# Performance work log

Measured on AMD Instinct MI355X. Metric: run time of the kernel, lower is better.

The kernel has to match this reference:

```python
import jax, jax.numpy as jnp
import numpy as np
from jax import lax

H = 128          # hidden_size
D = 8            # input_size
GX, GY = 4, 4    # grid_size
C = GX * GY      # grid cells
NS = 4.0         # neighborhood_size
T = 15           # obs_len
N = 16384        # neighbors per frame


def setup_inputs() -> dict:
    key = jax.random.key(0)
    ks = jax.random.split(key, 30)
    def w(i, shape):
        return jax.random.normal(ks[i], shape, jnp.float32) * 0.05
    return {
        "observed_trajectory_target": jax.random.normal(ks[0], (T, D), jnp.float32),
        "observed_trajectory_others": jax.random.normal(ks[1], (T, N, D), jnp.float32),
        "neighbor_mask": jax.random.randint(ks[2], (T, N), 0, 2, dtype=jnp.int32),
        "W_ih": w(3, (4 * H, D)), "W_hh": w(4, (4 * H, H)),
        "b_ih": w(5, (4 * H,)), "b_hh": w(6, (4 * H,)),
        "Wq": w(7, (H, H)), "bq": w(8, (H,)),
        "Wk": w(9, (H, H)), "bk": w(10, (H,)),
        "Wv": w(11, (H, H)), "bv": w(12, (H,)),
        "Wo": w(13, (H, H)), "bo": w(14, (H,)),
        "Wgq": w(15, (H, H)), "bgq": w(16, (H,)),
        "Wgk": w(17, (H, H)), "bgk": w(18, (H,)),
        "Wgv": w(19, (H, H)), "bgv": w(20, (H,)),
        "Wc": w(21, (2, H)), "bc": w(22, (2,)),
    }


def _lstm_cell(x, h, c, W_ih, W_hh, b_ih, b_hh):
    # torch LSTMCell gate order: i, f, g, o
    g = x @ W_ih.T + b_ih + h @ W_hh.T + b_hh
    i, f, gg, o = jnp.split(g, 4, axis=-1)
    c2 = jax.nn.sigmoid(f) * c + jax.nn.sigmoid(i) * jnp.tanh(gg)
    h2 = jax.nn.sigmoid(o) * jnp.tanh(c2)
    return h2, c2


def _forward(target, others, mask, W_ih, W_hh, b_ih, b_hh, Wq, bq, Wk, bk, Wv, bv,
             Wo, bo, Wgq, bgq, Wgk, bgk, Wgv, bgv, Wc, bc):
    # Neighbor LSTM is re-initialized to zero every timestep in the original
    # -> single LSTM step from zero state, vectorized over [T, N].
    g = jnp.einsum('tnd,kd->tnk', others, W_ih) + b_ih + b_hh
    i, f, gg, o = jnp.split(g, 4, axis=-1)
    c_o = jax.nn.sigmoid(i) * jnp.tanh(gg)
    h_others = jax.nn.sigmoid(o) * jnp.tanh(c_o)          # [T, N, H]

    scale = 1.0 / jnp.sqrt(jnp.asarray(H, jnp.float32))
    half = NS / 2.0
    cw, ch = NS / GX, NS / GY
    cells = jnp.arange(C, dtype=jnp.int32)

    def step(carry, xs):
        h, c = carry
        xt, ho, pos, mk = xs                               # [D], [N,H], [N,2], [N]
        h, c = _lstm_cell(xt[None, :], h, c, W_ih, W_hh, b_ih, b_hh)  # [1,H]
        # --- dynamic grid binning (trunc-toward-zero matches torch .long()) ---
        rel = pos - xt[:2]                                 # [N,2]
        in_nb = (jnp.abs(rel[:, 0]) <= half) & (jnp.abs(rel[:, 1]) <= half)
        cx = jnp.trunc(rel[:, 0] / cw).astype(jnp.int32) + GX // 2
        cy = jnp.trunc(rel[:, 1] / ch).astype(jnp.int32) + GY // 2
        valid = in_nb & (cx >= 0) & (cx < GX) & (cy >= 0) & (cy < GY) & (mk != 0)
        idx = cy * GX + cx                                 # [N]
        member = (idx[None, :] == cells[:, None]) & valid[None, :]  # [C,N]
        # --- per-cell single-query attention (1-head MHA) ---
        q = h @ Wq.T + bq                                  # [1,H]
        k = ho @ Wk.T + bk                                 # [N,H]
        v = ho @ Wv.T + bv                                 # [N,H]
        sc = (q @ k.T)[0] * scale                          # [N]
        mx = jnp.max(jnp.where(member, sc[None, :], -1e30), axis=1, keepdims=True)
        e = jnp.where(member, jnp.exp(sc[None, :] - mx), 0.0)
        w = e / jnp.maximum(e.sum(axis=1, keepdims=True), 1e-30)  # [C,N]
        nonempty = member.any(axis=1)                      # [C]
        cell_out = (w @ v) @ Wo.T + bo                     # [C,H]
        cell_out = jnp.where(nonempty[:, None], cell_out, 0.0)  # empty cells -> exact zeros
        # --- grid-level attention over the C cell summaries ---
        K = cell_out @ Wgk.T + bgk                         # [C,H]
        V = cell_out @ Wgv.T + bgv                         # [C,H]
        qg = h @ Wgq.T + bgq                               # [1,H]
        gw = jax.nn.softmax((qg @ K.T) * scale, axis=-1)   # [1,C]
        ctx = gw @ V                                       # [1,H]
        combined = h + ctx                                 # [1,H]
        return (h, c), combined

    h0 = jnp.zeros((1, H), jnp.float32)
    c0 = jnp.zeros((1, H), jnp.float32)
    _, ys = lax.scan(step, (h0, c0),
                     (target, h_others, others[..., :2], mask))
    combined = ys[-1][None]                                # [1,1,H] (matches torch broadcast)
    return combined @ Wc.T + bc                            # [1,1,2]


def reference(observed_trajectory_target, observed_trajectory_others, neighbor_mask,
              W_ih, W_hh, b_ih, b_hh, Wq, bq, Wk, bk, Wv, bv, Wo, bo,
              Wgq, bgq, Wgk, bgk, Wgv, bgv, Wc, bc):
    return _forward(observed_trajectory_target, observed_trajectory_others, neighbor_mask,
                    W_ih, W_hh, b_ih, b_hh, Wq, bq, Wk, bk, Wv, bv, Wo, bo,
                    Wgq, bgq, Wgk, bgk, Wgv, bgv, Wc, bc)
```

## Files before the change

### kernel.cpp

```cpp
#include <hip/hip_runtime.h>
#include <math.h>

#define WS_H     0
#define WS_U     128
#define WS_W2    256
#define WS_QBK   384
#define WS_S0    385
#define WS_S1    386
#define WS_GUARD 400
#define WS_ACCR  512
#define REP_STRIDE 2064
#define NREP 4

__device__ __forceinline__ float frcp_(float x){ return __builtin_amdgcn_rcpf(x); }
__device__ __forceinline__ float fsig_(float x){ return frcp_(1.f + __expf(-x)); }
__device__ __forceinline__ float ftanh_(float x){ return 1.f - 2.f*frcp_(1.f + __expf(2.f*x)); }

__device__ __forceinline__ float pf_(const float* __restrict__ p, int n, int part, int tid) {
    const int per4 = n >> 7;
    const float4* p4 = (const float4*)p + part * per4;
    float a = 0.f;
    for (int i = tid; i < per4; i += 256) { float4 v = p4[i]; a += v.x + v.y + v.z + v.w; }
    return a;
}

__global__ __launch_bounds__(256) void k0_prefetch(
    const float* __restrict__ W_ih, const float* __restrict__ W_hh,
    const float* __restrict__ Wq,  const float* __restrict__ Wk,
    const float* __restrict__ Wv,  const float* __restrict__ Wo,
    const float* __restrict__ Wgq, const float* __restrict__ Wgk,
    const float* __restrict__ Wgv, const float* __restrict__ Wc,
    float* __restrict__ ws)
{
    const int tid = threadIdx.x;
    const int bid = blockIdx.x;
    if (bid == 0) {
        for (int i = tid; i < NREP * REP_STRIDE; i += 256) ws[WS_ACCR + i] = 0.f;
    }
    const int part = bid >> 3;
    float a = pf_(W_hh, 65536, part, tid);
    a += pf_(W_ih, 4096,  part, tid);
    a += pf_(Wq,  16384, part, tid);
    a += pf_(Wk,  16384, part, tid);
    a += pf_(Wv,  16384, part, tid);
    a += pf_(Wo,  16384, part, tid);
    a += pf_(Wgq, 16384, part, tid);
    a += pf_(Wgk, 16384, part, tid);
    a += pf_(Wgv, 16384, part, tid);
    if (part < 2) a += pf_(Wc, 256, part, tid);
    if (a == 1.0e38f) ws[WS_GUARD] = a;
}

__global__ __launch_bounds__(512, 2) void k1_target(
    const float* __restrict__ target,
    const float* __restrict__ W_ih, const float* __restrict__ W_hh,
    const float* __restrict__ b_ih, const float* __restrict__ b_hh,
    const float* __restrict__ Wq,  const float* __restrict__ bq,
    const float* __restrict__ Wk,  const float* __restrict__ bk,
    const float* __restrict__ Wv,  const float* __restrict__ bv,
    const float* __restrict__ Wo,  const float* __restrict__ bo,
    const float* __restrict__ Wgq, const float* __restrict__ bgq,
    const float* __restrict__ Wgk, const float* __restrict__ bgk,
    float* __restrict__ ws)
{
    __shared__ __align__(16) float h_s[128];
    __shared__ float g_s[512];
    __shared__ float red[512];
    __shared__ __align__(16) float qq_s[256];
    __shared__ __align__(16) float u_s[128], ug_s[128], w1_s[128], w2_s[128];
    const int tid = threadIdx.x;
    if (tid < 128) h_s[tid] = 0.f;

    float wih[8];
    #pragma unroll
    for (int k = 0; k < 8; ++k) wih[k] = W_ih[tid*8 + k];
    const float bsum = b_ih[tid] + b_hh[tid];
    float4 whh[32];
    {
        const float4* w4 = (const float4*)(W_hh + tid*128);
        #pragma unroll
        for (int m = 0; m < 32; ++m) whh[m] = w4[m];
    }
    float c = 0.f;
    __syncthreads();

    for (int t = 0; t < 15; ++t) {
        float g = bsum;
        #pragma unroll
        for (int k = 0; k < 8; ++k) g += target[t*8 + k] * wih[k];
        const float4* h4 = (const float4*)h_s;
        float a0 = 0.f, a1 = 0.f, a2 = 0.f, a3 = 0.f;
        #pragma unroll
        for (int m = 0; m < 32; m += 4) {
            float4 x0 = h4[m], x1 = h4[m+1], x2 = h4[m+2], x3 = h4[m+3];
            a0 += whh[m  ].x*x0.x + whh[m  ].y*x0.y + whh[m  ].z*x0.z + whh[m  ].w*x0.w;
            a1 += whh[m+1].x*x1.x + whh[m+1].y*x1.y + whh[m+1].z*x1.z + whh[m+1].w*x1.w;
            a2 += whh[m+2].x*x2.x + whh[m+2].y*x2.y + whh[m+2].z*x2.z + whh[m+2].w*x2.w;
            a3 += whh[m+3].x*x3.x + whh[m+3].y*x3.y + whh[m+3].z*x3.z + whh[m+3].w*x3.w;
        }
        g += (a0 + a1) + (a2 + a3);
        g_s[tid] = g;
        __syncthreads();
        if (tid < 128) {
            float ig = fsig_(g_s[tid]);
            float fg = fsig_(g_s[tid+128]);
            float gg = ftanh_(g_s[tid+256]);
            float og = fsig_(g_s[tid+384]);
            c = fg*c + ig*gg;
            h_s[tid] = og*ftanh_(c);
        }
        __syncthreads();
    }

    {
        const int o = tid & 255, p = tid >> 8;
        const float* Wrow = (o < 128) ? (Wq + o*128) : (Wgq + (o & 127)*128);
        const float4* w4 = (const float4*)Wrow + p*16;
        const float4* h4 = (const float4*)h_s + p*16;
        float a = 0.f;
        #pragma unroll
        for (int m = 0; m < 16; ++m) { float4 w = w4[m], v = h4[m];
            a += w.x*v.x + w.y*v.y + w.z*v.z + w.w*v.w; }
        red[tid] = a;
    }
    __syncthreads();
    if (tid < 256) qq_s[tid] = red[tid] + red[tid+256] + ((tid < 128) ? bq[tid] : bgq[tid & 127]);
    __syncthreads();
    {
        const int o = tid & 255, p = tid >> 8;
        const int a_ = o & 127;
        const float* W = (o < 128) ? Wk : Wgk;
        const int qb = (o < 128) ? 0 : 128;
        float a = 0.f;
        #pragma unroll 8
        for (int j = p*64; j < p*64 + 64; ++j) a += qq_s[qb + j] * W[j*128 + a_];
        red[tid] = a;
    }
    __syncthreads();
    if (tid < 256) {
        float v = red[tid] + red[tid+256];
        if (tid < 128) u_s[tid] = v; else ug_s[tid & 127] = v;
    }
    __syncthreads();
    {
        const int o = tid & 127, p = tid >> 7;
        float a = 0.f;
        #pragma unroll 8
        for (int j = p*32; j < p*32 + 32; ++j) a += ug_s[j] * Wo[j*128 + o];
        red[tid] = a;
    }
    __syncthreads();
    if (tid < 128) w1_s[tid] = red[tid] + red[tid+128] + red[tid+256] + red[tid+384];
    __syncthreads();
    {
        const int o = tid & 127, p = tid >> 7;
        float a = 0.f;
        #pragma unroll 8
        for (int j = p*32; j < p*32 + 32; ++j) a += w1_s[j] * Wv[j*128 + o];
        red[tid] = a;
    }
    __syncthreads();
    if (tid < 128) w2_s[tid] = red[tid] + red[tid+128] + red[tid+256] + red[tid+384];
    __syncthreads();
    if (tid < 128) {
        red[tid]     = qq_s[tid] * bk[tid];
        red[128+tid] = qq_s[128+tid] * bgk[tid];
        red[256+tid] = w1_s[tid]*bv[tid] + ug_s[tid]*bo[tid];
    }
    __syncthreads();
    if (tid == 0) {
        float qbk = 0.f, s0 = 0.f, sx = 0.f;
        for (int j = 0; j < 128; ++j) { qbk += red[j]; s0 += red[128+j]; sx += red[256+j]; }
        ws[WS_QBK] = qbk; ws[WS_S0] = s0; ws[WS_S1] = sx + s0;
    }
    if (tid < 128) {
        ws[WS_H + tid]  = h_s[tid];
        ws[WS_U + tid]  = u_s[tid];
        ws[WS_W2 + tid] = w2_s[tid];
    }
}

#define K3_BLOCKS 64
__global__ __launch_bounds__(256) void k3_neighbors(
    const float* __restrict__ target, const float* __restrict__ others,
    const int* __restrict__ mask, const float* __restrict__ W_ih,
    const float* __restrict__ b_ih, const float* __restrict__ b_hh,
    float* __restrict__ ws)
{
    __shared__ float accs[16*128];
    __shared__ float esums[16];
    __shared__ int used[16];
    const int tid  = threadIdx.x;
    const int lane = tid & 63;
    const int wave = tid >> 6;

    for (int i = tid; i < 2048; i += 256) accs[i] = 0.f;
    if (tid < 16) { esums[tid] = 0.f; used[tid] = 0; }

    const int d0 = lane, d1 = lane + 64;
    float wi0[8], wg0[8], wo0[8], wi1[8], wg1[8], wo1[8];
    #pragma unroll
    for (int k = 0; k < 8; ++k) {
        wi0[k] = W_ih[d0*8+k];        wi1[k] = W_ih[d1*8+k];
        wg0[k] = W_ih[(256+d0)*8+k];  wg1[k] = W_ih[(256+d1)*8+k];
        wo0[k] = W_ih[(384+d0)*8+k];  wo1[k] = W_ih[(384+d1)*8+k];
    }
    const float bi0 = b_ih[d0]+b_hh[d0],         bi1 = b_ih[d1]+b_hh[d1];
    const float bg0 = b_ih[256+d0]+b_hh[256+d0], bg1 = b_ih[256+d1]+b_hh[256+d1];
    const float bo0 = b_ih[384+d0]+b_hh[384+d0], bo1 = b_ih[384+d1]+b_hh[384+d1];
    const float u0 = ws[WS_U + d0], u1 = ws[WS_U + d1];
    const float qbk = ws[WS_QBK];
    const float tx0 = target[14*8 + 0], tx1 = target[14*8 + 1];
    const float* __restrict__ oth  = others + 14*16384*8;
    const int*   __restrict__ mk14 = mask   + 14*16384;
    const float scale = 0.08838834764831845f;
    __syncthreads();

    const int gw = blockIdx.x*4 + wave;
    const int nper = 16384 / (K3_BLOCKS*4);
    for (int n = gw*nper; n < gw*nper + nper; ++n) {
        const int mk = mk14[n];
        const float4 xa = ((const float4*)oth)[n*2];
        const float4 xb = ((const float4*)oth)[n*2 + 1];
        const float r0 = xa.x - tx0, r1 = xa.y - tx1;
        bool ok = (fabsf(r0) <= 2.f) & (fabsf(r1) <= 2.f) & (mk != 0);
        const int cx = (int)truncf(r0) + 2;
        const int cy = (int)truncf(r1) + 2;
        ok = ok & (cx >= 0) & (cx < 4) & (cy >= 0) & (cy < 4);
        if (!ok) continue;
        const int cell = cy*4 + cx;
        float x[8] = {xa.x, xa.y, xa.z, xa.w, xb.x, xb.y, xb.z, xb.w};
        float gi = bi0, gg = bg0, go = bo0;
        #pragma unroll
        for (int k = 0; k < 8; ++k) { gi += x[k]*wi0[k]; gg += x[k]*wg0[k]; go += x[k]*wo0[k]; }
        const float ho0 = fsig_(go) * ftanh_(fsig_(gi) * ftanh_(gg));
        gi = bi1; gg = bg1; go = bo1;
        #pragma unroll
        for (int k = 0; k < 8; ++k) { gi += x[k]*wi1[k]; gg += x[k]*wg1[k]; go += x[k]*wo1[k]; }
        const float ho1 = fsig_(go) * ftanh_(fsig_(gi) * ftanh_(gg));
        float p = u0*ho0 + u1*ho1;
        #pragma unroll
        for (int s = 1; s < 64; s <<= 1) p += __shfl_xor(p, s, 64);
        const float sc = (p + qbk) * scale;
        const float e = __expf(sc);
        atomicAdd(&accs[cell*128 + d0], e*ho0);
        atomicAdd(&accs[cell*128 + d1], e*ho1);
        if (lane == 0) { atomicAdd(&esums[cell], e); used[cell] = 1; }
    }
    __syncthreads();
    const int rep = blockIdx.x & (NREP-1);
    float* wacc = ws + WS_ACCR + rep*REP_STRIDE;
    for (int i = tid; i < 2048; i += 256) {
        const int c = i >> 7;
        if (used[c]) {
            const float v = accs[i];
            if (v != 0.f) atomicAdd(&wacc[i], v);
        }
    }
    if (tid < 16 && used[tid]) atomicAdd(&wacc[2048 + tid], esums[tid]);
}

__global__ __launch_bounds__(128) void k4_finale(
    const float* __restrict__ Wv, const float* __restrict__ bv,
    const float* __restrict__ Wo, const float* __restrict__ bo,
    const float* __restrict__ Wgv, const float* __restrict__ bgv,
    const float* __restrict__ Wc, const float* __restrict__ bc,
    const float* __restrict__ ws, float* __restrict__ out)
{
    __shared__ __align__(16) float avg[16*128];
    __shared__ float es_s[16];
    __shared__ float gw_s[16];
    __shared__ float s_sh[16];
    __shared__ __align__(16) float mavg[128], t_s[128], mix[128], comb[128];
    __shared__ float alpha_s;
    const int tid = threadIdx.x;
    const float scale = 0.08838834764831845f;

    if (tid < 16) {
        float e = 0.f;
        #pragma unroll
        for (int r = 0; r < NREP; ++r) e += ws[WS_ACCR + r*REP_STRIDE + 2048 + tid];
        es_s[tid] = e;
    }
    __syncthreads();
    #pragma unroll
    for (int c = 0; c < 16; ++c) {
        float a = 0.f;
        #pragma unroll
        for (int r = 0; r < NREP; ++r) a += ws[WS_ACCR + r*REP_STRIDE + c*128 + tid];
        avg[c*128 + tid] = (es_s[c] > 0.f) ? a / es_s[c] : 0.f;
    }
    __syncthreads();
    if (tid < 16) {
        float s;
        if (es_s[tid] > 0.f) {
            s = ws[WS_S1];
            for (int m = 0; m < 128; ++m) s += ws[WS_W2 + m] * avg[tid*128 + m];
        } else {
            s = ws[WS_S0];
        }
        s_sh[tid] = s * scale;
    }
    __syncthreads();
    if (tid == 0) {
        float mx = -1e30f;
        #pragma unroll
        for (int c = 0; c < 16; ++c) mx = fmaxf(mx, s_sh[c]);
        float e[16]; float den = 0.f;
        #pragma unroll
        for (int c = 0; c < 16; ++c) { e[c] = __expf(s_sh[c] - mx); den += e[c]; }
        float a = 0.f;
        #pragma unroll
        for (int c = 0; c < 16; ++c) {
            const float g = e[c] / den;
            gw_s[c] = g;
            if (es_s[c] > 0.f) a += g;
        }
        alpha_s = a;
    }
    __syncthreads();
    {
        float a = 0.f;
        #pragma unroll
        for (int c = 0; c < 16; ++c) a += gw_s[c] * avg[c*128 + tid];
        mavg[tid] = a;
    }
    __syncthreads();
    const float alpha = alpha_s;
    {
        float a = alpha * bv[tid];
        const float4* w = (const float4*)(Wv + tid*128);
        const float4* v = (const float4*)mavg;
        #pragma unroll
        for (int m = 0; m < 32; ++m) { float4 ww = w[m], vv = v[m];
            a += ww.x*vv.x + ww.y*vv.y + ww.z*vv.z + ww.w*vv.w; }
        t_s[tid] = a;
    }
    __syncthreads();
    {
        float a = alpha * bo[tid];
        const float4* w = (const float4*)(Wo + tid*128);
        const float4* v = (const float4*)t_s;
        #pragma unroll
        for (int m = 0; m < 32; ++m) { float4 ww = w[m], vv = v[m];
            a += ww.x*vv.x + ww.y*vv.y + ww.z*vv.z + ww.w*vv.w; }
        mix[tid] = a;
    }
    __syncthreads();
    {
        float a = bgv[tid];
        const float4* w = (const float4*)(Wgv + tid*128);
        const float4* v = (const float4*)mix;
        #pragma unroll
        for (int m = 0; m < 32; ++m) { float4 ww = w[m], vv = v[m];
            a += ww.x*vv.x + ww.y*vv.y + ww.z*vv.z + ww.w*vv.w; }
        comb[tid] = ws[WS_H + tid] + a;
    }
    __syncthreads();
    if (tid < 2) {
        float a = bc[tid];
        for (int m = 0; m < 128; ++m) a += Wc[tid*128 + m] * comb[m];
        out[tid] = a;
    }
}

extern "C" void kernel_launch(void* const* d_in, const int* in_sizes, int n_in,
                              void* d_out, int out_size, void* d_ws, size_t ws_size,
                              hipStream_t stream) {
    (void)in_sizes; (void)n_in; (void)out_size; (void)ws_size;
    const float* target = (const float*)d_in[0];
    const float* others = (const float*)d_in[1];
    const int*   mask   = (const int*)d_in[2];
    const float* W_ih = (const float*)d_in[3];
    const float* W_hh = (const float*)d_in[4];
    const float* b_ih = (const float*)d_in[5];
    const float* b_hh = (const float*)d_in[6];
    const float* Wq  = (const float*)d_in[7];  const float* bq  = (const float*)d_in[8];
    const float* Wk  = (const float*)d_in[9];  const float* bk  = (const float*)d_in[10];
    const float* Wv  = (const float*)d_in[11]; const float* bv  = (const float*)d_in[12];
    const float* Wo  = (const float*)d_in[13]; const float* bo  = (const float*)d_in[14];
    const float* Wgq = (const float*)d_in[15]; const float* bgq = (const float*)d_in[16];
    const float* Wgk = (const float*)d_in[17]; const float* bgk = (const float*)d_in[18];
    const float* Wgv = (const float*)d_in[19]; const float* bgv = (const float*)d_in[20];
    const float* Wc  = (const float*)d_in[21]; const float* bc  = (const float*)d_in[22];
    float* ws  = (float*)d_ws;
    float* out = (float*)d_out;

    k0_prefetch<<<dim3(256), dim3(256), 0, stream>>>(W_ih, W_hh, Wq, Wk, Wv, Wo,
        Wgq, Wgk, Wgv, Wc, ws);
    k1_target<<<dim3(1), dim3(512), 0, stream>>>(target, W_ih, W_hh, b_ih, b_hh,
        Wq, bq, Wk, bk, Wv, bv, Wo, bo, Wgq, bgq, Wgk, bgk, ws);
    k3_neighbors<<<dim3(K3_BLOCKS), dim3(256), 0, stream>>>(target, others, mask,
        W_ih, b_ih, b_hh, ws);
    k4_finale<<<dim3(1), dim3(128), 0, stream>>>(Wv, bv, Wo, bo, Wgv, bgv, Wc, bc, ws, out);
}
```

Baseline: 189.1 us.

## Overlap neighbor LSTM with target recurrence in fused kernel, split accumulation pass

```diff
diff --git a/kernel.cpp b/kernel.cpp
--- a/kernel.cpp
+++ b/kernel.cpp
@@ -1,5 +1,8 @@
 #include <hip/hip_runtime.h>
 #include <math.h>
+
+#define NH 16384
+#define HDIM 128
 
 #define WS_H     0
 #define WS_U     128
@@ -8,51 +11,19 @@
 #define WS_S0    385
 #define WS_S1    386
 #define WS_GUARD 400
-#define WS_ACCR  512
+#define WS_CELL  512
+#define WS_ACCR  17408
 #define REP_STRIDE 2064
-#define NREP 4
+#define NREP 16
+#define WS_HO    65536
 
 __device__ __forceinline__ float frcp_(float x){ return __builtin_amdgcn_rcpf(x); }
 __device__ __forceinline__ float fsig_(float x){ return frcp_(1.f + __expf(-x)); }
 __device__ __forceinline__ float ftanh_(float x){ return 1.f - 2.f*frcp_(1.f + __expf(2.f*x)); }
 
-__device__ __forceinline__ float pf_(const float* __restrict__ p, int n, int part, int tid) {
-    const int per4 = n >> 7;
-    const float4* p4 = (const float4*)p + part * per4;
-    float a = 0.f;
-    for (int i = tid; i < per4; i += 256) { float4 v = p4[i]; a += v.x + v.y + v.z + v.w; }
-    return a;
-}
-
-__global__ __launch_bounds__(256) void k0_prefetch(
-    const float* __restrict__ W_ih, const float* __restrict__ W_hh,
-    const float* __restrict__ Wq,  const float* __restrict__ Wk,
-    const float* __restrict__ Wv,  const float* __restrict__ Wo,
-    const float* __restrict__ Wgq, const float* __restrict__ Wgk,
-    const float* __restrict__ Wgv, const float* __restrict__ Wc,
-    float* __restrict__ ws)
-{
-    const int tid = threadIdx.x;
-    const int bid = blockIdx.x;
-    if (bid == 0) {
-        for (int i = tid; i < NREP * REP_STRIDE; i += 256) ws[WS_ACCR + i] = 0.f;
-    }
-    const int part = bid >> 3;
-    float a = pf_(W_hh, 65536, part, tid);
-    a += pf_(W_ih, 4096,  part, tid);
-    a += pf_(Wq,  16384, part, tid);
-    a += pf_(Wk,  16384, part, tid);
-    a += pf_(Wv,  16384, part, tid);
-    a += pf_(Wo,  16384, part, tid);
-    a += pf_(Wgq, 16384, part, tid);
-    a += pf_(Wgk, 16384, part, tid);
-    a += pf_(Wgv, 16384, part, tid);
-    if (part < 2) a += pf_(Wc, 256, part, tid);
-    if (a == 1.0e38f) ws[WS_GUARD] = a;
-}
-
-__global__ __launch_bounds__(512, 2) void k1_target(
-    const float* __restrict__ target,
+__global__ __launch_bounds__(512, 2) void kI_fused(
+    const float* __restrict__ target, const float* __restrict__ others,
+    const int* __restrict__ mask,
     const float* __restrict__ W_ih, const float* __restrict__ W_hh,
     const float* __restrict__ b_ih, const float* __restrict__ b_hh,
     const float* __restrict__ Wq,  const float* __restrict__ bq,
@@ -61,14 +32,80 @@
     const float* __restrict__ Wo,  const float* __restrict__ bo,
     const float* __restrict__ Wgq, const float* __restrict__ bgq,
     const float* __restrict__ Wgk, const float* __restrict__ bgk,
+    const float* __restrict__ Wgv,
     float* __restrict__ ws)
 {
+    const int tid = threadIdx.x;
+    const int bid = blockIdx.x;
+
+    if (bid != 0) {
+        __shared__ float xs[64*8];
+        const int nb = bid - 1;
+        const int n0 = nb * 64;
+        const float* __restrict__ oth = others + 14*NH*8;
+
+        if (nb < NREP) {
+            float* g = ws + WS_ACCR + nb*REP_STRIDE;
+            for (int i = tid; i < REP_STRIDE; i += 512) g[i] = 0.f;
+        }
+        if ((bid & 7) == 0) {
+            const int m = (bid >> 3) - 1;
+            if (m < 7) {
+                const float* M = (m==0)?Wq:(m==1)?Wk:(m==2)?Wgq:(m==3)?Wgk:(m==4)?Wo:(m==5)?Wv:Wgv;
+                const float4* p4 = (const float4*)M;
+                float a = 0.f;
+                for (int i = tid; i < 4096; i += 512) { float4 v = p4[i]; a += v.x+v.y+v.z+v.w; }
+                if (a == 1.0e38f) ws[WS_GUARD] = a;
+            }
+        }
+
+        for (int i = tid; i < 512; i += 512) xs[i] = oth[n0*8 + i];
+
+        const int d = tid & 127;
+        const int sub = tid >> 7;
+        float wi[8], wg[8], wo[8];
+        #pragma unroll
+        for (int k = 0; k < 8; ++k) {
+            wi[k] = W_ih[d*8 + k];
+            wg[k] = W_ih[(256+d)*8 + k];
+            wo[k] = W_ih[(384+d)*8 + k];
+        }
+        const float bi  = b_ih[d]     + b_hh[d];
+        const float bg  = b_ih[256+d] + b_hh[256+d];
+        const float bo_ = b_ih[384+d] + b_hh[384+d];
+        __syncthreads();
+
+        if (tid < 64) {
+            const int n = n0 + tid;
+            const float tx0 = target[14*8 + 0], tx1 = target[14*8 + 1];
+            const float r0 = xs[tid*8]     - tx0;
+            const float r1 = xs[tid*8 + 1] - tx1;
+            bool ok = (fabsf(r0) <= 2.f) & (fabsf(r1) <= 2.f) & (mask[14*NH + n] != 0);
+            const int cx = (int)truncf(r0) + 2;
+            const int cy = (int)truncf(r1) + 2;
+            ok = ok & (cx >= 0) & (cx < 4) & (cy >= 0) & (cy < 4);
+            ((int*)(ws + WS_CELL))[n] = ok ? (cy*4 + cx) : -1;
+        }
+
+        float* __restrict__ hoq = ws + WS_HO;
+        #pragma unroll 4
+        for (int p = 0; p < 16; ++p) {
+            const int j = sub + 4*p;
+            const float* x = &xs[j*8];
+            float gi = bi, gg = bg, go = bo_;
+            #pragma unroll
+            for (int k = 0; k < 8; ++k) { gi += x[k]*wi[k]; gg += x[k]*wg[k]; go += x[k]*wo[k]; }
+            const float ho = fsig_(go) * ftanh_(fsig_(gi) * ftanh_(gg));
+            hoq[(n0 + j)*128 + d] = ho;
+        }
+        return;
+    }
+
     __shared__ __align__(16) float h_s[128];
     __shared__ float g_s[512];
     __shared__ float red[512];
     __shared__ __align__(16) float qq_s[256];
     __shared__ __align__(16) float u_s[128], ug_s[128], w1_s[128], w2_s[128];
-    const int tid = threadIdx.x;
     if (tid < 128) h_s[tid] = 0.f;
 
     float wih[8];
@@ -180,97 +217,56 @@
     }
 }
 
-#define K3_BLOCKS 64
-__global__ __launch_bounds__(256) void k3_neighbors(
-    const float* __restrict__ target, const float* __restrict__ others,
-    const int* __restrict__ mask, const float* __restrict__ W_ih,
-    const float* __restrict__ b_ih, const float* __restrict__ b_hh,
-    float* __restrict__ ws)
+__global__ __launch_bounds__(256) void kII_accum(float* __restrict__ ws)
 {
-    __shared__ float accs[16*128];
-    __shared__ float esums[16];
-    __shared__ int used[16];
+    __shared__ float acc[REP_STRIDE];
     const int tid  = threadIdx.x;
     const int lane = tid & 63;
-    const int wave = tid >> 6;
-
-    for (int i = tid; i < 2048; i += 256) accs[i] = 0.f;
-    if (tid < 16) { esums[tid] = 0.f; used[tid] = 0; }
-
-    const int d0 = lane, d1 = lane + 64;
-    float wi0[8], wg0[8], wo0[8], wi1[8], wg1[8], wo1[8];
-    #pragma unroll
-    for (int k = 0; k < 8; ++k) {
-        wi0[k] = W_ih[d0*8+k];        wi1[k] = W_ih[d1*8+k];
-        wg0[k] = W_ih[(256+d0)*8+k];  wg1[k] = W_ih[(256+d1)*8+k];
-        wo0[k] = W_ih[(384+d0)*8+k];  wo1[k] = W_ih[(384+d1)*8+k];
-    }
-    const float bi0 = b_ih[d0]+b_hh[d0],         bi1 = b_ih[d1]+b_hh[d1];
-    const float bg0 = b_ih[256+d0]+b_hh[256+d0], bg1 = b_ih[256+d1]+b_hh[256+d1];
-    const float bo0 = b_ih[384+d0]+b_hh[384+d0], bo1 = b_ih[384+d1]+b_hh[384+d1];
-    const float u0 = ws[WS_U + d0], u1 = ws[WS_U + d1];
+    const int wv   = tid >> 6;
+
+    for (int i = tid; i < REP_STRIDE; i += 256) acc[i] = 0.f;
+
+    const float u0 = ws[WS_U + lane];
+    const float u1 = ws[WS_U + 64 + lane];
     const float qbk = ws[WS_QBK];
-    const float tx0 = target[14*8 + 0], tx1 = target[14*8 + 1];
-    const float* __restrict__ oth  = others + 14*16384*8;
-    const int*   __restrict__ mk14 = mask   + 14*16384;
     const float scale = 0.08838834764831845f;
-    __syncthreads();
-
-    const int gw = blockIdx.x*4 + wave;
-    const int nper = 16384 / (K3_BLOCKS*4);
-    for (int n = gw*nper; n < gw*nper + nper; ++n) {
-        const int mk = mk14[n];
-        const float4 xa = ((const float4*)oth)[n*2];
-        const float4 xb = ((const float4*)oth)[n*2 + 1];
-        const float r0 = xa.x - tx0, r1 = xa.y - tx1;
-        bool ok = (fabsf(r0) <= 2.f) & (fabsf(r1) <= 2.f) & (mk != 0);
-        const int cx = (int)truncf(r0) + 2;
-        const int cy = (int)truncf(r1) + 2;
-        ok = ok & (cx >= 0) & (cx < 4) & (cy >= 0) & (cy < 4);
-        if (!ok) continue;
-        const int cell = cy*4 + cx;
-        float x[8] = {xa.x, xa.y, xa.z, xa.w, xb.x, xb.y, xb.z, xb.w};
-        float gi = bi0, gg = bg0, go = bo0;
-        #pragma unroll
-        for (int k = 0; k < 8; ++k) { gi += x[k]*wi0[k]; gg += x[k]*wg0[k]; go += x[k]*wo0[k]; }
-        const float ho0 = fsig_(go) * ftanh_(fsig_(gi) * ftanh_(gg));
-        gi = bi1; gg = bg1; go = bo1;
-        #pragma unroll
-        for (int k = 0; k < 8; ++k) { gi += x[k]*wi1[k]; gg += x[k]*wg1[k]; go += x[k]*wo1[k]; }
-        const float ho1 = fsig_(go) * ftanh_(fsig_(gi) * ftanh_(gg));
-        float p = u0*ho0 + u1*ho1;
+    const float* __restrict__ hoq = ws + WS_HO;
+    const int* __restrict__ cellw = (const int*)(ws + WS_CELL);
+    __syncthreads();
+
+    const int n0 = blockIdx.x*64 + wv*16;
+    #pragma unroll 2
+    for (int i = 0; i < 16; ++i) {
+        const int n = n0 + i;
+        const int cw = cellw[n];
+        const float h0 = hoq[n*128 + lane];
+        const float h1 = hoq[n*128 + 64 + lane];
+        float p = u0*h0 + u1*h1;
         #pragma unroll
         for (int s = 1; s < 64; s <<= 1) p += __shfl_xor(p, s, 64);
-        const float sc = (p + qbk) * scale;
-        const float e = __expf(sc);
-        atomicAdd(&accs[cell*128 + d0], e*ho0);
-        atomicAdd(&accs[cell*128 + d1], e*ho1);
-        if (lane == 0) { atomicAdd(&esums[cell], e); used[cell] = 1; }
-    }
-    __syncthreads();
-    const int rep = blockIdx.x & (NREP-1);
-    float* wacc = ws + WS_ACCR + rep*REP_STRIDE;
-    for (int i = tid; i < 2048; i += 256) {
-        const int c = i >> 7;
-        if (used[c]) {
-            const float v = accs[i];
-            if (v != 0.f) atomicAdd(&wacc[i], v);
-        }
-    }
-    if (tid < 16 && used[tid]) atomicAdd(&wacc[2048 + tid], esums[tid]);
+        const float e = (cw >= 0) ? __expf((p + qbk) * scale) : 0.f;
+        const int cell = (cw >= 0) ? cw : 0;
+        atomicAdd(&acc[cell*128 + lane], e*h0);
+        atomicAdd(&acc[cell*128 + 64 + lane], e*h1);
+        if (lane == 0) atomicAdd(&acc[2048 + cell], e);
+    }
+    __syncthreads();
+    float* g = ws + WS_ACCR + (blockIdx.x & (NREP-1))*REP_STRIDE;
+    for (int i = tid; i < REP_STRIDE; i += 256) {
+        const float v = acc[i];
+        if (v != 0.f) atomicAdd(&g[i], v);
+    }
 }
 
-__global__ __launch_bounds__(128) void k4_finale(
+__global__ __launch_bounds__(256) void kIII_finale(
     const float* __restrict__ Wv, const float* __restrict__ bv,
     const float* __restrict__ Wo, const float* __restrict__ bo,
     const float* __restrict__ Wgv, const float* __restrict__ bgv,
     const float* __restrict__ Wc, const float* __restrict__ bc,
     const float* __restrict__ ws, float* __restrict__ out)
 {
-    __shared__ __align__(16) float avg[16*128];
-    __shared__ float es_s[16];
-    __shared__ float gw_s[16];
-    __shared__ float s_sh[16];
+    __shared__ __align__(16) float avg[2048];
+    __shared__ float es_s[16], gw_s[16], s_sh[16];
     __shared__ __align__(16) float mavg[128], t_s[128], mix[128], comb[128];
     __shared__ float alpha_s;
     const int tid = threadIdx.x;
@@ -283,23 +279,26 @@
         es_s[tid] = e;
     }
     __syncthreads();
-    #pragma unroll
-    for (int c = 0; c < 16; ++c) {
-        float a = 0.f;
-        #pragma unroll
-        for (int r = 0; r < NREP; ++r) a += ws[WS_ACCR + r*REP_STRIDE + c*128 + tid];
-        avg[c*128 + tid] = (es_s[c] > 0.f) ? a / es_s[c] : 0.f;
-    }
-    __syncthreads();
-    if (tid < 16) {
-        float s;
-        if (es_s[tid] > 0.f) {
-            s = ws[WS_S1];
-            for (int m = 0; m < 128; ++m) s += ws[WS_W2 + m] * avg[tid*128 + m];
-        } else {
-            s = ws[WS_S0];
-        }
-        s_sh[tid] = s * scale;
+    for (int i = tid; i < 2048; i += 256) {
+        float a = 0.f;
+        #pragma unroll
+        for (int r = 0; r < NREP; ++r) a += ws[WS_ACCR + r*REP_STRIDE + i];
+        const float es = es_s[i >> 7];
+        avg[i] = (es > 0.f) ? a / es : 0.f;
+    }
+    __syncthreads();
+    if (tid < 128) {
+        const int c = tid >> 3, j = tid & 7;
+        float a = 0.f;
+        #pragma unroll
+        for (int k = 0; k < 16; ++k) {
+            const int d = j + 8*k;
+            a += ws[WS_W2 + d] * avg[c*128 + d];
+        }
+        #pragma unroll
+        for (int s = 1; s < 8; s <<= 1) a += __shfl_xor(a, s, 64);
+        if (j == 0)
+            s_sh[c] = ((es_s[c] > 0.f) ? (ws[WS_S1] + a) : ws[WS_S0]) * scale;
     }
     __syncthreads();
     if (tid == 0) {
@@ -319,7 +318,7 @@
         alpha_s = a;
     }
     __syncthreads();
-    {
+    if (tid < 128) {
         float a = 0.f;
         #pragma unroll
         for (int c = 0; c < 16; ++c) a += gw_s[c] * avg[c*128 + tid];
@@ -327,7 +326,7 @@
     }
     __syncthreads();
     const float alpha = alpha_s;
-    {
+    if (tid < 128) {
         float a = alpha * bv[tid];
         const float4* w = (const float4*)(Wv + tid*128);
         const float4* v = (const float4*)mavg;
@@ -337,7 +336,7 @@
         t_s[tid] = a;
     }
     __syncthreads();
-    {
+    if (tid < 128) {
         float a = alpha * bo[tid];
         const float4* w = (const float4*)(Wo + tid*128);
         const float4* v = (const float4*)t_s;
@@ -347,7 +346,7 @@
         mix[tid] = a;
     }
     __syncthreads();
-    {
+    if (tid < 128) {
         float a = bgv[tid];
         const float4* w = (const float4*)(Wgv + tid*128);
         const float4* v = (const float4*)mix;
@@ -386,11 +385,10 @@
     float* ws  = (float*)d_ws;
     float* out = (float*)d_out;
 
-    k0_prefetch<<<dim3(256), dim3(256), 0, stream>>>(W_ih, W_hh, Wq, Wk, Wv, Wo,
-        Wgq, Wgk, Wgv, Wc, ws);
-    k1_target<<<dim3(1), dim3(512), 0, stream>>>(target, W_ih, W_hh, b_ih, b_hh,
-        Wq, bq, Wk, bk, Wv, bv, Wo, bo, Wgq, bgq, Wgk, bgk, ws);
-    k3_neighbors<<<dim3(K3_BLOCKS), dim3(256), 0, stream>>>(target, others, mask,
-        W_ih, b_ih, b_hh, ws);
-    k4_finale<<<dim3(1), dim3(128), 0, stream>>>(Wv, bv, Wo, bo, Wgv, bgv, Wc, bc, ws, out);
+    kI_fused<<<dim3(257), dim3(512), 0, stream>>>(target, others, mask,
+        W_ih, W_hh, b_ih, b_hh, Wq, bq, Wk, bk, Wv, bv, Wo, bo,
+        Wgq, bgq, Wgk, bgk, Wgv, ws);
+    kII_accum<<<dim3(256), dim3(256), 0, stream>>>(ws);
+    kIII_finale<<<dim3(1), dim3(256), 0, stream>>>(Wv, bv, Wo, bo, Wgv, bgv,
+        Wc, bc, ws, out);
 }
```

After: 167.4 us. 1.13x faster.
